# Kernel tuning notes

Measured on AMD Instinct MI355X. Metric: run time of the kernel, lower is better.

The kernel has to match this reference:

```python
import jax, jax.numpy as jnp
import numpy as np

B_, DIM, NPTS = 16, 128, 16384
J, K, L = 16, 128, 128   # kernel_mode, GkNN_mode_out, GkNN_mode_in
R, M1, M2 = 8, 64, 64    # low-rank A/B dims and mask modes


def setup_inputs() -> dict:
    key = jax.random.key(0)
    ks = jax.random.split(key, 9)
    scale = 1.0 / (L * K)
    return {
        "x": jax.random.normal(ks[0], (B_, DIM, NPTS), jnp.float32),
        "bases": jax.random.normal(ks[1], (NPTS, K), jnp.float32),
        "wbases": jax.random.normal(ks[2], (NPTS, L), jnp.float32),
        "product": jax.random.normal(ks[3], (K, L), jnp.float32),
        "D_out": jax.random.normal(ks[4], (J, K), jnp.float32),
        "D_in": jax.random.normal(ks[5], (J, L), jnp.float32),
        "A": jax.random.normal(ks[6], (J, R, M1), jnp.float32),
        "B": jax.random.normal(ks[7], (J, R, M2), jnp.float32),
        "weights": scale * jax.random.normal(ks[8], (DIM, DIM, J), jnp.float32),
    }


def reference(x, bases, wbases, product, D_out, D_in, A, B, weights):
    # project onto weighted bases: (b, c, npts) @ (npts, L) -> (b, c, L)
    x_hat = jnp.einsum('bcx,xl->bcl', x, wbases)
    # H tensor: (J, K, L) broadcast product + low-rank correction
    H = D_out[:, :, None] * D_in[:, None, :] * product[None, :, :]
    Q = jnp.einsum('jrm,jrn->jmn', A, B)  # bmm(A^T, B): (J, M1, M2)
    H = H.at[:, :Q.shape[1], :Q.shape[2]].add(Q)
    # mode mixing: (J,K,L) x (b,i,L) -> (b,i,J,K), then weights (i,o,J)
    x_hat1 = jnp.einsum('jkl,bil->bijk', H, x_hat)
    y = jnp.einsum('ioj,bijk->bok', weights, x_hat1)
    # back to physical space: (b, o, K) x (npts, K) -> (b, o, npts)
    return jnp.einsum('bok,xk->box', y, bases)
```

## Files before the change

### kernel.cpp

```cpp
#include <hip/hip_runtime.h>

#define B_    16
#define DIM   128
#define NPTS  16384
#define J_    16
#define K_    128
#define L_    128
#define R_    8
#define M1_   64

typedef float  f32x4 __attribute__((ext_vector_type(4)));
typedef short  s16x8 __attribute__((ext_vector_type(8)));
typedef unsigned short u16;
typedef u16 u16x8 __attribute__((ext_vector_type(8)));
typedef u16 u16x4 __attribute__((ext_vector_type(4)));

__device__ __forceinline__ u16 f2bf(float f) {
    unsigned u = __float_as_uint(f);
    u += 0x7FFFu + ((u >> 16) & 1u);
    return (u16)(u >> 16);
}
#define MFMA16(a,b,c) __builtin_amdgcn_mfma_f32_16x16x32_bf16((a),(b),(c),0,0,0)

#define OFF_R0   0u
#define OFF_R1   8388608u
#define OFF_HKL  12582912u
#define OFF_W2T  13107200u
#define OFF_XHB  13631488u
#define OFF_YB   14155776u
#define OFF_YP   14680064u

__global__ __launch_bounds__(128) void k_prep(
    const float* __restrict__ product, const float* __restrict__ Do,
    const float* __restrict__ Di, const float* __restrict__ A,
    const float* __restrict__ Bm, const float* __restrict__ W,
    u16* __restrict__ Hkl, u16* __restrict__ W2T)
{
    int bid = blockIdx.x, t = threadIdx.x;
    if (bid < 2048) {
        int j = bid >> 7, k = bid & 127, l = t;
        float v = Do[j*K_ + k] * Di[j*L_ + l] * product[k*L_ + l];
        if (k < M1_ && l < M1_) {
            float q = 0.f;
            #pragma unroll
            for (int r = 0; r < R_; ++r)
                q += A[(j*R_ + r)*M1_ + k] * Bm[(j*R_ + r)*M1_ + l];
            v += q;
        }
        Hkl[j*16384 + k*128 + l] = f2bf(v);
    } else {
        int idx = (bid - 2048)*128 + t;
        int o = idx >> 11, ji = idx & 2047, j = ji >> 7, i = ji & 127;
        W2T[idx] = f2bf(W[(i*DIM + o)*J_ + j]);
    }
}

__global__ __launch_bounds__(256) void k_wbT(
    const float* __restrict__ wb, u16* __restrict__ wbT)
{
    __shared__ u16 sT[128][136];
    const int t = threadIdx.x, p0 = blockIdx.x * 128;
    #pragma unroll
    for (int it = 0; it < 16; ++it) {
        int idx = it*256 + t, row = idx >> 5, c4 = (idx & 31) * 4;
        float4 v = *(const float4*)(wb + (size_t)(p0+row)*L_ + c4);
        sT[c4+0][row] = f2bf(v.x); sT[c4+1][row] = f2bf(v.y);
        sT[c4+2][row] = f2bf(v.z); sT[c4+3][row] = f2bf(v.w);
    }
    __syncthreads();
    #pragma unroll
    for (int it = 0; it < 8; ++it) {
        int idx = it*256 + t, l = idx >> 4, pc = (idx & 15) * 8;
        *(u16x8*)(wbT + (size_t)l*NPTS + p0 + pc) = *(const u16x8*)&sT[l][pc];
    }
}

__global__ __launch_bounds__(256) void k_cvt(
    const float* __restrict__ s, u16* __restrict__ d)
{
    int i = (blockIdx.x*256 + threadIdx.x) * 4;
    float4 v = *(const float4*)(s + i);
    u16x4 o = { f2bf(v.x), f2bf(v.y), f2bf(v.z), f2bf(v.w) };
    *(u16x4*)(d + i) = o;
}

__global__ __launch_bounds__(512) void k_stageA(
    const float* __restrict__ x, const u16* __restrict__ wbT,
    float* __restrict__ part)
{
    __shared__ u16 sA[64][72];
    __shared__ u16 sB[128][72];
    const int t = threadIdx.x, lane = t & 63, wave = t >> 6;
    const int quad = lane >> 4, l16 = lane & 15;
    const int wr = wave >> 2, wc = wave & 3;
    const int m0 = blockIdx.x * 64;
    const size_t pbase = (size_t)blockIdx.y * 2048;

    f32x4 acc[2][2] = {};
    const int ac4 = (t & 15) * 4, arr = t >> 4;
    const int bc8 = (t & 7) * 8,  brr = t >> 3;

    for (int pc = 0; pc < 2048; pc += 64) {
        #pragma unroll
        for (int i = 0; i < 2; ++i) {
            int row = arr + 32*i;
            float4 v = *(const float4*)(x + (size_t)(m0+row)*NPTS + pbase + pc + ac4);
            u16x4 h = { f2bf(v.x), f2bf(v.y), f2bf(v.z), f2bf(v.w) };
            *(u16x4*)&sA[row][ac4] = h;
        }
        #pragma unroll
        for (int i = 0; i < 2; ++i) {
            int row = brr + 64*i;
            *(u16x8*)&sB[row][bc8] =
                *(const u16x8*)(wbT + (size_t)row*NPTS + pbase + pc + bc8);
        }
        __syncthreads();
        #pragma unroll
        for (int ks = 0; ks < 2; ++ks) {
            int kb = ks*32 + quad*8;
            s16x8 a0 = *(const s16x8*)&sA[wr*32      + l16][kb];
            s16x8 a1 = *(const s16x8*)&sA[wr*32 + 16 + l16][kb];
            s16x8 b0 = *(const s16x8*)&sB[wc*32      + l16][kb];
            s16x8 b1 = *(const s16x8*)&sB[wc*32 + 16 + l16][kb];
            acc[0][0] = MFMA16(a0, b0, acc[0][0]);
            acc[0][1] = MFMA16(a0, b1, acc[0][1]);
            acc[1][0] = MFMA16(a1, b0, acc[1][0]);
            acc[1][1] = MFMA16(a1, b1, acc[1][1]);
        }
        __syncthreads();
    }
    float* po = part + (size_t)blockIdx.y * (2048*128);
    #pragma unroll
    for (int mt = 0; mt < 2; ++mt)
      #pragma unroll
      for (int r = 0; r < 4; ++r) {
        int row = m0 + wr*32 + mt*16 + quad*4 + r;
        #pragma unroll
        for (int nt = 0; nt < 2; ++nt) {
            int col = wc*32 + nt*16 + l16;
            po[(size_t)row*128 + col] = acc[mt][nt][r];
        }
      }
}

__global__ __launch_bounds__(256) void k_reduceA(
    const float* __restrict__ part, u16* __restrict__ xhatb)
{
    int i = blockIdx.x * 1024 + threadIdx.x;
    #pragma unroll
    for (int e = 0; e < 4; ++e, i += 256) {
        float s = 0.f;
        #pragma unroll
        for (int p = 0; p < 8; ++p) s += part[p*262144 + i];
        xhatb[i] = f2bf(s);
    }
}

__global__ __launch_bounds__(256) void k_mix1(
    const u16* __restrict__ Hkl, const u16* __restrict__ xhatb,
    u16* __restrict__ Tt)
{
    __shared__ u16 sA[128][136];
    __shared__ u16 sB[128][136];
    const int t = threadIdx.x, lane = t & 63, wave = t >> 6;
    const int quad = lane >> 4, l16 = lane & 15;
    const int wr = wave >> 1, wc = wave & 1;
    const int b = blockIdx.x, j = blockIdx.y;
    const u16* ha = Hkl + j*16384;
    const u16* xb = xhatb + b*16384;

    const int c8 = (t & 15)*8, rr = t >> 4;
    #pragma unroll
    for (int i = 0; i < 8; ++i) {
        int row = rr + 16*i;
        *(u16x8*)&sA[row][c8] = *(const u16x8*)(ha + row*128 + c8);
        *(u16x8*)&sB[row][c8] = *(const u16x8*)(xb + row*128 + c8);
    }
    __syncthreads();

    f32x4 acc[4][4] = {};
    #pragma unroll
    for (int ks = 0; ks < 4; ++ks) {
        int kb = ks*32 + quad*8;
        s16x8 a[4], bf[4];
        #pragma unroll
        for (int mt = 0; mt < 4; ++mt) a[mt]  = *(const s16x8*)&sA[wr*64 + mt*16 + l16][kb];
        #pragma unroll
        for (int nt = 0; nt < 4; ++nt) bf[nt] = *(const s16x8*)&sB[wc*64 + nt*16 + l16][kb];
        #pragma unroll
        for (int mt = 0; mt < 4; ++mt)
            #pragma unroll
            for (int nt = 0; nt < 4; ++nt)
                acc[mt][nt] = MFMA16(a[mt], bf[nt], acc[mt][nt]);
    }
    u16* to = Tt + (size_t)b*262144 + (j << 7);
    #pragma unroll
    for (int mt = 0; mt < 4; ++mt)
      #pragma unroll
      for (int r = 0; r < 4; ++r) {
        int k = wr*64 + mt*16 + quad*4 + r;
        #pragma unroll
        for (int nt = 0; nt < 4; ++nt) {
            int i = wc*64 + nt*16 + l16;
            to[(size_t)k*2048 + i] = f2bf(acc[mt][nt][r]);
        }
      }
}

__global__ __launch_bounds__(256) void k_mix2(
    const u16* __restrict__ W2T, const u16* __restrict__ Tt,
    float* __restrict__ ypart)
{
    __shared__ u16 sA[128][72];
    __shared__ u16 sB[128][72];
    const int t = threadIdx.x, lane = t & 63, wave = t >> 6;
    const int quad = lane >> 4, l16 = lane & 15;
    const int wr = wave >> 1, wc = wave & 1;
    const int b = blockIdx.x, js = blockIdx.y;
    const int ji0 = js * 512;
    const u16* tb = Tt + (size_t)b*262144;

    f32x4 acc[4][4] = {};
    const int c8 = (t & 7)*8, rr = t >> 3;
    for (int pc = 0; pc < 512; pc += 64) {
        #pragma unroll
        for (int i = 0; i < 4; ++i) {
            int row = rr + 32*i;
            *(u16x8*)&sA[row][c8] = *(const u16x8*)(W2T + (size_t)row*2048 + ji0 + pc + c8);
            *(u16x8*)&sB[row][c8] = *(const u16x8*)(tb  + (size_t)row*2048 + ji0 + pc + c8);
        }
        __syncthreads();
        #pragma unroll
        for (int ks = 0; ks < 2; ++ks) {
            int kb = ks*32 + quad*8;
            s16x8 a[4], bf[4];
            #pragma unroll
            for (int mt = 0; mt < 4; ++mt) a[mt]  = *(const s16x8*)&sA[wr*64 + mt*16 + l16][kb];
            #pragma unroll
            for (int nt = 0; nt < 4; ++nt) bf[nt] = *(const s16x8*)&sB[wc*64 + nt*16 + l16][kb];
            #pragma unroll
            for (int mt = 0; mt < 4; ++mt)
                #pragma unroll
                for (int nt = 0; nt < 4; ++nt)
                    acc[mt][nt] = MFMA16(a[mt], bf[nt], acc[mt][nt]);
        }
        __syncthreads();
    }
    float* yo = ypart + ((size_t)(js*16 + b) << 14);
    #pragma unroll
    for (int mt = 0; mt < 4; ++mt)
      #pragma unroll
      for (int r = 0; r < 4; ++r) {
        int o = wr*64 + mt*16 + quad*4 + r;
        #pragma unroll
        for (int nt = 0; nt < 4; ++nt) {
            int k = wc*64 + nt*16 + l16;
            yo[(size_t)o*128 + k] = acc[mt][nt][r];
        }
      }
}

__global__ __launch_bounds__(256) void k_reduceY(
    const float* __restrict__ part, u16* __restrict__ yb)
{
    int i = blockIdx.x * 1024 + threadIdx.x;
    #pragma unroll
    for (int e = 0; e < 4; ++e, i += 256) {
        float s = part[i] + part[262144 + i] + part[2*262144 + i] + part[3*262144 + i];
        yb[i] = f2bf(s);
    }
}

__global__ __launch_bounds__(256) void k_stageE(
    const u16* __restrict__ yb, const u16* __restrict__ basesb,
    float* __restrict__ out)
{
    __shared__ u16 sA[128][136];
    __shared__ u16 sB[128][136];
    const int t = threadIdx.x, lane = t & 63, wave = t >> 6;
    const int quad = lane >> 4, l16 = lane & 15;
    const int wr = wave >> 1, wc = wave & 1;
    const int bo0 = blockIdx.x * 128, p0 = blockIdx.y * 128;

    const int c8 = (t & 15)*8, rr = t >> 4;
    #pragma unroll
    for (int i = 0; i < 8; ++i) {
        int row = rr + 16*i;
        *(u16x8*)&sA[row][c8] = *(const u16x8*)(yb     + (size_t)(bo0+row)*128 + c8);
        *(u16x8*)&sB[row][c8] = *(const u16x8*)(basesb + (size_t)(p0 +row)*128 + c8);
    }
    __syncthreads();

    f32x4 acc[4][4] = {};
    #pragma unroll
    for (int ks = 0; ks < 4; ++ks) {
        int kb = ks*32 + quad*8;
        s16x8 a[4], bf[4];
        #pragma unroll
        for (int mt = 0; mt < 4; ++mt) a[mt]  = *(const s16x8*)&sA[wr*64 + mt*16 + l16][kb];
        #pragma unroll
        for (int nt = 0; nt < 4; ++nt) bf[nt] = *(const s16x8*)&sB[wc*64 + nt*16 + l16][kb];
        #pragma unroll
        for (int mt = 0; mt < 4; ++mt)
            #pragma unroll
            for (int nt = 0; nt < 4; ++nt)
                acc[mt][nt] = MFMA16(a[mt], bf[nt], acc[mt][nt]);
    }
    #pragma unroll
    for (int mt = 0; mt < 4; ++mt)
      #pragma unroll
      for (int r = 0; r < 4; ++r) {
        size_t row = bo0 + wr*64 + mt*16 + quad*4 + r;
        #pragma unroll
        for (int nt = 0; nt < 4; ++nt) {
            int p = p0 + wc*64 + nt*16 + l16;
            out[row*NPTS + p] = acc[mt][nt][r];
        }
      }
}

extern "C" void kernel_launch(void* const* d_in, const int* in_sizes, int n_in,
                              void* d_out, int out_size, void* d_ws, size_t ws_size,
                              hipStream_t stream) {
    (void)in_sizes; (void)n_in; (void)out_size; (void)ws_size;
    const float* x       = (const float*)d_in[0];
    const float* bases   = (const float*)d_in[1];
    const float* wbases  = (const float*)d_in[2];
    const float* product = (const float*)d_in[3];
    const float* Do      = (const float*)d_in[4];
    const float* Di      = (const float*)d_in[5];
    const float* A       = (const float*)d_in[6];
    const float* Bm      = (const float*)d_in[7];
    const float* W       = (const float*)d_in[8];

    char* ws = (char*)d_ws;
    float* partA  = (float*)(ws + OFF_R0);
    u16*   Tt     = (u16*)  (ws + OFF_R0);
    u16*   wbT    = (u16*)  (ws + OFF_R1);
    u16*   basesb = (u16*)  (ws + OFF_R1);
    u16*   Hkl    = (u16*)  (ws + OFF_HKL);
    u16*   W2T    = (u16*)  (ws + OFF_W2T);
    u16*   xhatb  = (u16*)  (ws + OFF_XHB);
    u16*   yb     = (u16*)  (ws + OFF_YB);
    float* ypart  = (float*)(ws + OFF_YP);

    k_prep   <<<4096, 128, 0, stream>>>(product, Do, Di, A, Bm, W, Hkl, W2T);
    k_wbT    <<<128, 256, 0, stream>>>(wbases, wbT);
    k_stageA <<<dim3(32, 8), 512, 0, stream>>>(x, wbT, partA);
    k_reduceA<<<256, 256, 0, stream>>>(partA, xhatb);
    k_cvt    <<<2048, 256, 0, stream>>>(bases, basesb);
    k_mix1   <<<dim3(16, 16), 256, 0, stream>>>(Hkl, xhatb, Tt);
    k_mix2   <<<dim3(16, 4), 256, 0, stream>>>(W2T, Tt, ypart);
    k_reduceY<<<256, 256, 0, stream>>>(ypart, yb);
    k_stageE <<<dim3(16, 128), 256, 0, stream>>>(yb, basesb, (float*)d_out);
}
```

Baseline: 317.5 us.

## Fuse prep kernels, widen stageA K-tile, split mix2 reduction across more blocks

Merges the H/W2 prep, wbases transpose and bases bf16 conversion into one k_prep launch, with separate workspace regions so nothing is overwritten. This removes two launches. k_stageA now loads 128-wide K chunks per iteration, halving the barrier count at the cost of more LDS. k_mix2 now runs 16x16 blocks that each handle a single 128-wide ji chunk, raising parallelism from 64 blocks, so k_reduceY sums 16 partials instead of 4 and adds more partial-buffer traffic.

```diff
diff --git a/kernel.cpp b/kernel.cpp
--- a/kernel.cpp
+++ b/kernel.cpp
@@ -22,23 +22,28 @@
 }
 #define MFMA16(a,b,c) __builtin_amdgcn_mfma_f32_16x16x32_bf16((a),(b),(c),0,0,0)
 
-#define OFF_R0   0u
-#define OFF_R1   8388608u
-#define OFF_HKL  12582912u
-#define OFF_W2T  13107200u
-#define OFF_XHB  13631488u
-#define OFF_YB   14155776u
-#define OFF_YP   14680064u
-
-__global__ __launch_bounds__(128) void k_prep(
+#define OFF_PARTA 0u
+#define OFF_WBT   8388608u
+#define OFF_BASB  12582912u
+#define OFF_HKL   16777216u
+#define OFF_W2T   17301504u
+#define OFF_XHB   17825792u
+#define OFF_YB    18350080u
+#define OFF_YP    18874368u
+
+__global__ __launch_bounds__(256) void k_prep(
     const float* __restrict__ product, const float* __restrict__ Do,
     const float* __restrict__ Di, const float* __restrict__ A,
     const float* __restrict__ Bm, const float* __restrict__ W,
-    u16* __restrict__ Hkl, u16* __restrict__ W2T)
-{
-    int bid = blockIdx.x, t = threadIdx.x;
-    if (bid < 2048) {
-        int j = bid >> 7, k = bid & 127, l = t;
+    const float* __restrict__ wb, const float* __restrict__ bases,
+    u16* __restrict__ Hkl, u16* __restrict__ W2T,
+    u16* __restrict__ wbT, u16* __restrict__ basesb)
+{
+    __shared__ u16 sT[128][136];
+    const int bid = blockIdx.x, t = threadIdx.x;
+    if (bid < 1024) {
+        int idx = (bid << 8) | t;
+        int j = idx >> 14, k = (idx >> 7) & 127, l = idx & 127;
         float v = Do[j*K_ + k] * Di[j*L_ + l] * product[k*L_ + l];
         if (k < M1_ && l < M1_) {
             float q = 0.f;
@@ -47,49 +52,40 @@
                 q += A[(j*R_ + r)*M1_ + k] * Bm[(j*R_ + r)*M1_ + l];
             v += q;
         }
-        Hkl[j*16384 + k*128 + l] = f2bf(v);
-    } else {
-        int idx = (bid - 2048)*128 + t;
+        Hkl[idx] = f2bf(v);
+    } else if (bid < 2048) {
+        int idx = ((bid - 1024) << 8) | t;
         int o = idx >> 11, ji = idx & 2047, j = ji >> 7, i = ji & 127;
         W2T[idx] = f2bf(W[(i*DIM + o)*J_ + j]);
-    }
-}
-
-__global__ __launch_bounds__(256) void k_wbT(
-    const float* __restrict__ wb, u16* __restrict__ wbT)
-{
-    __shared__ u16 sT[128][136];
-    const int t = threadIdx.x, p0 = blockIdx.x * 128;
-    #pragma unroll
-    for (int it = 0; it < 16; ++it) {
-        int idx = it*256 + t, row = idx >> 5, c4 = (idx & 31) * 4;
-        float4 v = *(const float4*)(wb + (size_t)(p0+row)*L_ + c4);
-        sT[c4+0][row] = f2bf(v.x); sT[c4+1][row] = f2bf(v.y);
-        sT[c4+2][row] = f2bf(v.z); sT[c4+3][row] = f2bf(v.w);
-    }
-    __syncthreads();
-    #pragma unroll
-    for (int it = 0; it < 8; ++it) {
-        int idx = it*256 + t, l = idx >> 4, pc = (idx & 15) * 8;
-        *(u16x8*)(wbT + (size_t)l*NPTS + p0 + pc) = *(const u16x8*)&sT[l][pc];
-    }
-}
-
-__global__ __launch_bounds__(256) void k_cvt(
-    const float* __restrict__ s, u16* __restrict__ d)
-{
-    int i = (blockIdx.x*256 + threadIdx.x) * 4;
-    float4 v = *(const float4*)(s + i);
-    u16x4 o = { f2bf(v.x), f2bf(v.y), f2bf(v.z), f2bf(v.w) };
-    *(u16x4*)(d + i) = o;
+    } else if (bid < 2176) {
+        const int p0 = (bid - 2048) * 128;
+        #pragma unroll
+        for (int it = 0; it < 16; ++it) {
+            int idx = it*256 + t, row = idx >> 5, c4 = (idx & 31) * 4;
+            float4 v = *(const float4*)(wb + (size_t)(p0+row)*L_ + c4);
+            sT[c4+0][row] = f2bf(v.x); sT[c4+1][row] = f2bf(v.y);
+            sT[c4+2][row] = f2bf(v.z); sT[c4+3][row] = f2bf(v.w);
+        }
+        __syncthreads();
+        #pragma unroll
+        for (int it = 0; it < 8; ++it) {
+            int idx = it*256 + t, l = idx >> 4, pc = (idx & 15) * 8;
+            *(u16x8*)(wbT + (size_t)l*NPTS + p0 + pc) = *(const u16x8*)&sT[l][pc];
+        }
+    } else {
+        int i = (((bid - 2176) << 8) | t) * 4;
+        float4 v = *(const float4*)(bases + i);
+        u16x4 o4 = { f2bf(v.x), f2bf(v.y), f2bf(v.z), f2bf(v.w) };
+        *(u16x4*)(basesb + i) = o4;
+    }
 }
 
 __global__ __launch_bounds__(512) void k_stageA(
     const float* __restrict__ x, const u16* __restrict__ wbT,
     float* __restrict__ part)
 {
-    __shared__ u16 sA[64][72];
-    __shared__ u16 sB[128][72];
+    __shared__ u16 sA[64][136];
+    __shared__ u16 sB[128][136];
     const int t = threadIdx.x, lane = t & 63, wave = t >> 6;
     const int quad = lane >> 4, l16 = lane & 15;
     const int wr = wave >> 2, wc = wave & 3;
@@ -97,26 +93,26 @@
     const size_t pbase = (size_t)blockIdx.y * 2048;
 
     f32x4 acc[2][2] = {};
-    const int ac4 = (t & 15) * 4, arr = t >> 4;
-    const int bc8 = (t & 7) * 8,  brr = t >> 3;
-
-    for (int pc = 0; pc < 2048; pc += 64) {
-        #pragma unroll
-        for (int i = 0; i < 2; ++i) {
-            int row = arr + 32*i;
+    const int ac4 = (t & 31) * 4, arr = t >> 5;
+    const int bc8 = (t & 15) * 8, brr = t >> 4;
+
+    for (int pc = 0; pc < 2048; pc += 128) {
+        #pragma unroll
+        for (int i = 0; i < 4; ++i) {
+            int row = arr + 16*i;
             float4 v = *(const float4*)(x + (size_t)(m0+row)*NPTS + pbase + pc + ac4);
             u16x4 h = { f2bf(v.x), f2bf(v.y), f2bf(v.z), f2bf(v.w) };
             *(u16x4*)&sA[row][ac4] = h;
         }
         #pragma unroll
-        for (int i = 0; i < 2; ++i) {
-            int row = brr + 64*i;
+        for (int i = 0; i < 4; ++i) {
+            int row = brr + 32*i;
             *(u16x8*)&sB[row][bc8] =
                 *(const u16x8*)(wbT + (size_t)row*NPTS + pbase + pc + bc8);
         }
         __syncthreads();
         #pragma unroll
-        for (int ks = 0; ks < 2; ++ks) {
+        for (int ks = 0; ks < 4; ++ks) {
             int kb = ks*32 + quad*8;
             s16x8 a0 = *(const s16x8*)&sA[wr*32      + l16][kb];
             s16x8 a1 = *(const s16x8*)&sA[wr*32 + 16 + l16][kb];
@@ -211,42 +207,40 @@
     const u16* __restrict__ W2T, const u16* __restrict__ Tt,
     float* __restrict__ ypart)
 {
-    __shared__ u16 sA[128][72];
-    __shared__ u16 sB[128][72];
+    __shared__ u16 sA[128][136];
+    __shared__ u16 sB[128][136];
     const int t = threadIdx.x, lane = t & 63, wave = t >> 6;
     const int quad = lane >> 4, l16 = lane & 15;
     const int wr = wave >> 1, wc = wave & 1;
-    const int b = blockIdx.x, js = blockIdx.y;
-    const int ji0 = js * 512;
+    const int b = blockIdx.x, c = blockIdx.y;
+    const int ji0 = c * 128;
     const u16* tb = Tt + (size_t)b*262144;
 
+    const int c8 = (t & 15)*8, rr = t >> 4;
+    #pragma unroll
+    for (int i = 0; i < 8; ++i) {
+        int row = rr + 16*i;
+        *(u16x8*)&sA[row][c8] = *(const u16x8*)(W2T + (size_t)row*2048 + ji0 + c8);
+        *(u16x8*)&sB[row][c8] = *(const u16x8*)(tb  + (size_t)row*2048 + ji0 + c8);
+    }
+    __syncthreads();
+
     f32x4 acc[4][4] = {};
-    const int c8 = (t & 7)*8, rr = t >> 3;
-    for (int pc = 0; pc < 512; pc += 64) {
-        #pragma unroll
-        for (int i = 0; i < 4; ++i) {
-            int row = rr + 32*i;
-            *(u16x8*)&sA[row][c8] = *(const u16x8*)(W2T + (size_t)row*2048 + ji0 + pc + c8);
-            *(u16x8*)&sB[row][c8] = *(const u16x8*)(tb  + (size_t)row*2048 + ji0 + pc + c8);
-        }
-        __syncthreads();
-        #pragma unroll
-        for (int ks = 0; ks < 2; ++ks) {
-            int kb = ks*32 + quad*8;
-            s16x8 a[4], bf[4];
+    #pragma unroll
+    for (int ks = 0; ks < 4; ++ks) {
+        int kb = ks*32 + quad*8;
+        s16x8 a[4], bf[4];
+        #pragma unroll
+        for (int mt = 0; mt < 4; ++mt) a[mt]  = *(const s16x8*)&sA[wr*64 + mt*16 + l16][kb];
+        #pragma unroll
+        for (int nt = 0; nt < 4; ++nt) bf[nt] = *(const s16x8*)&sB[wc*64 + nt*16 + l16][kb];
+        #pragma unroll
+        for (int mt = 0; mt < 4; ++mt)
             #pragma unroll
-            for (int mt = 0; mt < 4; ++mt) a[mt]  = *(const s16x8*)&sA[wr*64 + mt*16 + l16][kb];
-            #pragma unroll
-            for (int nt = 0; nt < 4; ++nt) bf[nt] = *(const s16x8*)&sB[wc*64 + nt*16 + l16][kb];
-            #pragma unroll
-            for (int mt = 0; mt < 4; ++mt)
-                #pragma unroll
-                for (int nt = 0; nt < 4; ++nt)
-                    acc[mt][nt] = MFMA16(a[mt], bf[nt], acc[mt][nt]);
-        }
-        __syncthreads();
-    }
-    float* yo = ypart + ((size_t)(js*16 + b) << 14);
+            for (int nt = 0; nt < 4; ++nt)
+                acc[mt][nt] = MFMA16(a[mt], bf[nt], acc[mt][nt]);
+    }
+    float* yo = ypart + ((size_t)(c*16 + b) << 14);
     #pragma unroll
     for (int mt = 0; mt < 4; ++mt)
       #pragma unroll
@@ -266,7 +260,9 @@
     int i = blockIdx.x * 1024 + threadIdx.x;
     #pragma unroll
     for (int e = 0; e < 4; ++e, i += 256) {
-        float s = part[i] + part[262144 + i] + part[2*262144 + i] + part[3*262144 + i];
+        float s = 0.f;
+        #pragma unroll
+        for (int p = 0; p < 16; ++p) s += part[p*262144 + i];
         yb[i] = f2bf(s);
     }
 }
@@ -334,23 +330,22 @@
     const float* W       = (const float*)d_in[8];
 
     char* ws = (char*)d_ws;
-    float* partA  = (float*)(ws + OFF_R0);
-    u16*   Tt     = (u16*)  (ws + OFF_R0);
-    u16*   wbT    = (u16*)  (ws + OFF_R1);
-    u16*   basesb = (u16*)  (ws + OFF_R1);
+    float* partA  = (float*)(ws + OFF_PARTA);
+    u16*   Tt     = (u16*)  (ws + OFF_PARTA);
+    u16*   wbT    = (u16*)  (ws + OFF_WBT);
+    u16*   basesb = (u16*)  (ws + OFF_BASB);
     u16*   Hkl    = (u16*)  (ws + OFF_HKL);
     u16*   W2T    = (u16*)  (ws + OFF_W2T);
     u16*   xhatb  = (u16*)  (ws + OFF_XHB);
     u16*   yb     = (u16*)  (ws + OFF_YB);
     float* ypart  = (float*)(ws + OFF_YP);
 
-    k_prep   <<<4096, 128, 0, stream>>>(product, Do, Di, A, Bm, W, Hkl, W2T);
-    k_wbT    <<<128, 256, 0, stream>>>(wbases, wbT);
+    k_prep   <<<4224, 256, 0, stream>>>(product, Do, Di, A, Bm, W, wbases, bases,
+                                        Hkl, W2T, wbT, basesb);
     k_stageA <<<dim3(32, 8), 512, 0, stream>>>(x, wbT, partA);
     k_reduceA<<<256, 256, 0, stream>>>(partA, xhatb);
-    k_cvt    <<<2048, 256, 0, stream>>>(bases, basesb);
     k_mix1   <<<dim3(16, 16), 256, 0, stream>>>(Hkl, xhatb, Tt);
-    k_mix2   <<<dim3(16, 4), 256, 0, stream>>>(W2T, Tt, ypart);
+    k_mix2   <<<dim3(16, 16), 256, 0, stream>>>(W2T, Tt, ypart);
     k_reduceY<<<256, 256, 0, stream>>>(ypart, yb);
     k_stageE <<<dim3(16, 128), 256, 0, stream>>>(yb, basesb, (float*)d_out);
 }
```

New measurement: 315.6 us. About the same (-0.6%).
